# Optimization experiments

Hardware: AMD Instinct MI355X
Metric: run time of the kernel (lower is better)

Reference implementation:

```python
import jax, jax.numpy as jnp
import numpy as np

D_MODEL = 2048
N_HEADS = 8
EXPAND_K = 1
EXPAND_V = 2
DK = D_MODEL * EXPAND_K // N_HEADS      # 256 per-head key dim
DV = D_MODEL * EXPAND_V // N_HEADS      # 512 per-head value dim
INTER = 5632
EPS = 1e-6
CHUNK = 64


def setup_inputs() -> dict:
    key = jax.random.key(0)
    ks = jax.random.split(key, 12)
    d = D_MODEL
    s = lambda fan_in: 1.0 / np.sqrt(fan_in)
    return {
        "hidden_states": jax.random.normal(ks[0], (2, 2048, d), jnp.float32),
        "attn_norm_w": jnp.ones((d,), jnp.float32),
        "q_w": jax.random.normal(ks[1], (d, d * EXPAND_K), jnp.float32) * s(d),
        "k_w": jax.random.normal(ks[2], (d, d * EXPAND_K), jnp.float32) * s(d),
        "v_w": jax.random.normal(ks[3], (d, d * EXPAND_V), jnp.float32) * s(d),
        "g_w": jax.random.normal(ks[4], (d, d * EXPAND_V), jnp.float32) * s(d),
        "o_w": jax.random.normal(ks[5], (d * EXPAND_V, d), jnp.float32) * s(d * EXPAND_V),
        "gnorm_w": jnp.ones((DV,), jnp.float32),
        "mlp_norm_w": jnp.ones((d,), jnp.float32),
        "gate_w": jax.random.normal(ks[6], (d, INTER * 2), jnp.float32) * s(d),
        "down_w": jax.random.normal(ks[7], (INTER, d), jnp.float32) * s(INTER),
    }


def rmsnorm(x, w, eps=EPS):
    return x * jax.lax.rsqrt(jnp.mean(x * x, axis=-1, keepdims=True) + eps) * w


def rope(x):
    # x: [B, T, H, D]; non-interleaved rotary on full head dim
    T, D = x.shape[1], x.shape[-1]
    inv_freq = 1.0 / (10000.0 ** (jnp.arange(0, D, 2, dtype=jnp.float32) / D))
    ang = jnp.arange(T, dtype=jnp.float32)[:, None] * inv_freq  # [T, D/2]
    cos = jnp.cos(ang)[None, :, None, :]
    sin = jnp.sin(ang)[None, :, None, :]
    x1, x2 = jnp.split(x, 2, axis=-1)
    return jnp.concatenate([x1 * cos - x2 * sin, x2 * cos + x1 * sin], axis=-1)


def chunk_retention(q, k, v):
    # q,k: [B,T,H,Dk], v: [B,T,H,Dv]; chunkwise-recurrent RetNet retention
    B, T, H, Dk = q.shape
    Dv = v.shape[-1]
    C = CHUNK
    N = T // C
    gamma = 1.0 - jnp.exp2(-5.0 - jnp.arange(H, dtype=jnp.float32))  # [H]
    i = jnp.arange(C, dtype=jnp.float32)
    diff = i[:, None] - i[None, :]
    Dmask = jnp.where(diff >= 0, gamma[:, None, None] ** diff, 0.0)   # [H,C,C]
    cross_decay = gamma[:, None] ** (i[None, :] + 1.0)                # [H,C]
    k_decay = gamma[:, None] ** (C - 1.0 - i[None, :])                # [H,C]
    chunk_decay = gamma ** C                                          # [H]

    # -> [N, B, H, C, D]
    to_chunks = lambda x: jnp.moveaxis(
        x.reshape(B, N, C, H, x.shape[-1]).transpose(0, 1, 3, 2, 4), 1, 0)
    qc, kc, vc = to_chunks(q), to_chunks(k), to_chunks(v)

    def body(S, inp):
        qb, kb, vb = inp  # [B,H,C,Dk/Dv]
        attn = jnp.einsum('bhid,bhjd->bhij', qb, kb) * Dmask
        o_intra = jnp.einsum('bhij,bhje->bhie', attn, vb)
        o_cross = jnp.einsum('bhid,bhde->bhie', qb * cross_decay[None, :, :, None], S)
        S = chunk_decay[None, :, None, None] * S + \
            jnp.einsum('bhid,bhie->bhde', kb * k_decay[None, :, :, None], vb)
        return S, o_intra + o_cross

    S0 = jnp.zeros((B, H, Dk, Dv), q.dtype)
    _, o = jax.lax.scan(body, S0, (qc, kc, vc))  # o: [N,B,H,C,Dv]
    return jnp.moveaxis(o, 0, 1).transpose(0, 1, 3, 2, 4).reshape(B, T, H, Dv)


def reference(hidden_states, attn_norm_w, q_w, k_w, v_w, g_w, o_w, gnorm_w,
              mlp_norm_w, gate_w, down_w):
    B, T, d = hidden_states.shape
    residual = hidden_states
    h = rmsnorm(hidden_states, attn_norm_w)

    # MultiScaleRetention
    q = (h @ q_w).reshape(B, T, N_HEADS, DK)
    k = (h @ k_w).reshape(B, T, N_HEADS, DK)
    v = (h @ v_w).reshape(B, T, N_HEADS, DV)
    g = (h @ g_w).reshape(B, T, N_HEADS, DV)
    q, k = rope(q), rope(k)
    q = q * (DK ** -0.5)
    o = chunk_retention(q, k, v)
    # fused RMSNorm + swish gate (per head over Dv)
    o = rmsnorm(o, gnorm_w) * (g * jax.nn.sigmoid(g))
    h = o.reshape(B, T, N_HEADS * DV) @ o_w

    # fused-residual RMSNorm
    residual = h + residual
    h = rmsnorm(residual, mlp_norm_w)

    # SwiGLU MLP
    y = h @ gate_w
    gate, y = jnp.split(y, 2, axis=-1)
    h = (gate * jax.nn.sigmoid(gate) * y) @ down_w
    return residual + h
```

## Files before the change

### kernel.cpp

```cpp
#include <hip/hip_runtime.h>
#include <cstdint>
#include <cstddef>

typedef unsigned short u16;
typedef __attribute__((ext_vector_type(4))) float f32x4;
typedef __attribute__((ext_vector_type(4))) unsigned int u32x4;

__device__ __forceinline__ float b2f(u16 u) {
  union { unsigned int i; float f; } x; x.i = ((unsigned int)u) << 16; return x.f;
}
__device__ __forceinline__ u16 f2b(float f) {
  union { float f; unsigned int i; } x; x.f = f;
  unsigned int i = x.i;
  i += 0x7fffu + ((i >> 16) & 1u);
  return (u16)(i >> 16);
}

__device__ __forceinline__ void mfma_bf16(f32x4& c, u32x4 a, u32x4 b) {
  asm("v_mfma_f32_16x16x32_bf16 %0, %1, %2, %0" : "+v"(c) : "v"(a), "v"(b));
}

__device__ __forceinline__ void async_ld16(const u16* g, u16* l) {
  typedef __attribute__((address_space(1))) const unsigned int GU;
  typedef __attribute__((address_space(3))) unsigned int LU;
  __builtin_amdgcn_global_load_lds((GU*)g, (LU*)l, 16, 0, 0);
}

__global__ __launch_bounds__(256)
void transpose_cast_kernel(const float* __restrict__ in, u16* __restrict__ out,
                           int K, int N, int ldin) {
  __shared__ float tile[64][65];
  const int nb = N >> 6;
  const int bk = blockIdx.x / nb, bn = blockIdx.x % nb;
  const int k0 = bk * 64, n0 = bn * 64;
  const int tid = threadIdx.x;
#pragma unroll
  for (int p = 0; p < 16; ++p) {
    int idx = p * 256 + tid;
    int r = idx >> 6, c = idx & 63;
    tile[r][c] = in[(size_t)(k0 + r) * ldin + n0 + c];
  }
  __syncthreads();
#pragma unroll
  for (int p = 0; p < 16; ++p) {
    int idx = p * 256 + tid;
    int r = idx >> 6, c = idx & 63;
    out[(size_t)(n0 + r) * K + k0 + c] = f2b(tile[c][r]);
  }
}

__global__ __launch_bounds__(256)
void transpose_k_kernel(const u16* __restrict__ kb, u16* __restrict__ kt) {
  __shared__ u16 tile[64][72];
  const int bid = blockIdx.x;
  const int dd = bid & 3, tt = (bid >> 2) & 31;
  const int h = (bid >> 7) & 7, b = bid >> 10;
  const int t0 = tt * 64, d0 = dd * 64;
  const int tid = threadIdx.x;
#pragma unroll
  for (int p = 0; p < 2; ++p) {
    int idx = p * 256 + tid;
    int r = idx >> 3, cq = (idx & 7) * 8;
    *(uint4*)&tile[r][cq] =
        *(const uint4*)&kb[(size_t)(b * 2048 + t0 + r) * 2048 + h * 256 + d0 + cq];
  }
  __syncthreads();
#pragma unroll
  for (int p = 0; p < 2; ++p) {
    int idx = p * 256 + tid;
    int r = idx >> 3, cq = (idx & 7) * 8;
    union { u16 h8[8]; uint4 v4; } o;
#pragma unroll
    for (int j = 0; j < 8; ++j) o.h8[j] = tile[cq + j][r];
    *(uint4*)&kt[((size_t)(b * 8 + h) * 256 + d0 + r) * 2048 + t0 + cq] = o.v4;
  }
}

__global__ __launch_bounds__(256)
void rmsnorm_cast_kernel(const float* __restrict__ x, const float* __restrict__ w,
                         u16* __restrict__ out) {
  const int row = blockIdx.x, tid = threadIdx.x;
  const float* xr = x + (size_t)row * 2048;
  float4 a = ((const float4*)xr)[tid * 2];
  float4 b = ((const float4*)xr)[tid * 2 + 1];
  float ss = a.x*a.x + a.y*a.y + a.z*a.z + a.w*a.w
           + b.x*b.x + b.y*b.y + b.z*b.z + b.w*b.w;
#pragma unroll
  for (int m = 32; m; m >>= 1) ss += __shfl_xor(ss, m);
  __shared__ float ps[4];
  if ((tid & 63) == 0) ps[tid >> 6] = ss;
  __syncthreads();
  const float sc = rsqrtf((ps[0] + ps[1] + ps[2] + ps[3]) * (1.0f / 2048.0f) + 1e-6f);
  const int base = tid * 8;
  const float vals[8] = {a.x, a.y, a.z, a.w, b.x, b.y, b.z, b.w};
  union { u16 h[8]; uint4 v4[2]; } o;
#pragma unroll
  for (int j = 0; j < 8; ++j) o.h[j] = f2b(vals[j] * sc * w[base + j]);
  *(uint4*)&out[(size_t)row * 2048 + base] = o.v4[0];
  *(uint4*)&out[(size_t)row * 2048 + base + 8] = o.v4[1];
}

__global__ __launch_bounds__(256)
void rmsnorm_bf16_kernel(const u16* __restrict__ x, const float* __restrict__ w,
                         u16* __restrict__ out) {
  const int row = blockIdx.x, tid = threadIdx.x;
  union { uint4 v4; u16 h[8]; } p;
  p.v4 = *(const uint4*)&x[(size_t)row * 2048 + tid * 8];
  float v[8];
  float ss = 0.f;
#pragma unroll
  for (int j = 0; j < 8; ++j) { v[j] = b2f(p.h[j]); ss += v[j] * v[j]; }
#pragma unroll
  for (int m = 32; m; m >>= 1) ss += __shfl_xor(ss, m);
  __shared__ float ps[4];
  if ((tid & 63) == 0) ps[tid >> 6] = ss;
  __syncthreads();
  const float sc = rsqrtf((ps[0] + ps[1] + ps[2] + ps[3]) * (1.0f / 2048.0f) + 1e-6f);
  union { u16 h[8]; uint4 v4; } o;
#pragma unroll
  for (int j = 0; j < 8; ++j) o.h[j] = f2b(v[j] * sc * w[tid * 8 + j]);
  *(uint4*)&out[(size_t)row * 2048 + tid * 8] = o.v4;
}

__global__ __launch_bounds__(256)
void rope_table_kernel(float* __restrict__ ct, float* __restrict__ st) {
  const int idx = blockIdx.x * 256 + threadIdx.x;
  const int t = idx >> 7, i = idx & 127;
  const float e = -(float)i * (0.0078125f * log2f(10000.0f));
  const float ang = (float)t * exp2f(e);
  ct[idx] = cosf(ang);
  st[idx] = sinf(ang);
}

__global__ __launch_bounds__(256)
void rope_apply_kernel(u16* __restrict__ x, const float* __restrict__ ct,
                       const float* __restrict__ st, float scale) {
  const int gid = blockIdx.x * 256 + threadIdx.x;
  const int r = gid >> 8;
  const int rem = gid & 255;
  const int h = rem >> 5;
  const int i4 = (rem & 31) * 4;
  const int t = r & 2047;
  const size_t o1 = (size_t)r * 2048 + h * 256 + i4;
  union { ushort4 v; u16 h4[4]; } p1, p2, q1, q2;
  p1.v = *(ushort4*)&x[o1];
  p2.v = *(ushort4*)&x[o1 + 128];
  const float4 c = *(const float4*)&ct[t * 128 + i4];
  const float4 s = *(const float4*)&st[t * 128 + i4];
  const float cc[4] = {c.x, c.y, c.z, c.w};
  const float sn[4] = {s.x, s.y, s.z, s.w};
#pragma unroll
  for (int j = 0; j < 4; ++j) {
    float x1 = b2f(p1.h4[j]), x2 = b2f(p2.h4[j]);
    q1.h4[j] = f2b((x1 * cc[j] - x2 * sn[j]) * scale);
    q2.h4[j] = f2b((x2 * cc[j] + x1 * sn[j]) * scale);
  }
  *(ushort4*)&x[o1] = q1.v;
  *(ushort4*)&x[o1 + 128] = q2.v;
}

template <int BM, int EPI>
__global__ __launch_bounds__(512, 2)
void gemm2(const u16* __restrict__ A, const u16* __restrict__ Bt,
           void* Cout, const float* fsrc, const u16* hsrc, int N, int K) {
  constexpr int MF = BM / 32;
  constexpr int WROWS = BM / 2;
  constexpr int LA = BM / 128;
  constexpr int SLOTA = BM * 32;
  constexpr int SLOTB = 256 * 32;
  constexpr int SLOT = SLOTA + SLOTB;
  constexpr int VM2 = 2 * (LA + 2);
  __shared__ __align__(16) u16 lds[4 * SLOT];

  const int tid = threadIdx.x;
  const int l = tid & 63, w = tid >> 6;
  const int lr = l & 15, hi = l >> 4;
  const int wm = w >> 2, wn = w & 3;
  const int nbn = N >> 8;
  int bid;
  { int cpx = (int)gridDim.x >> 3; int ob = blockIdx.x;
    bid = (ob & 7) * cpx + (ob >> 3); }
  const int bm = bid / nbn, bn = bid % nbn;
  const int nt = K >> 5;

  size_t asrc[LA]; int adst[LA];
#pragma unroll
  for (int t = 0; t < LA; ++t) {
    int gi = t * 512 + tid;
    int row = gi >> 2;
    int ch = (gi & 3) ^ (row & 3);
    asrc[t] = (size_t)(bm * BM + row) * K + ch * 8;
    adst[t] = (t * 512 + w * 64) * 8;
  }
  size_t bsrc[2]; int bdst[2];
#pragma unroll
  for (int t = 0; t < 2; ++t) {
    int gi = t * 512 + tid;
    int row = gi >> 2;
    int ch = (gi & 3) ^ (row & 3);
    bsrc[t] = (size_t)(bn * 256 + row) * K + ch * 8;
    bdst[t] = SLOTA + (t * 512 + w * 64) * 8;
  }
  const int xch = (hi ^ (lr & 3)) << 3;
  int aoff[MF], boff[4];
#pragma unroll
  for (int m = 0; m < MF; ++m)
    aoff[m] = (wm * WROWS + m * 16 + lr) * 32 + xch;
#pragma unroll
  for (int n = 0; n < 4; ++n)
    boff[n] = SLOTA + (wn * 64 + n * 16 + lr) * 32 + xch;

  f32x4 acc[MF][4];
#pragma unroll
  for (int m = 0; m < MF; ++m)
#pragma unroll
    for (int n = 0; n < 4; ++n) acc[m][n] = (f32x4){0.f, 0.f, 0.f, 0.f};

  auto stage = [&](int kt, int s) {
    const int sb = s * SLOT;
#pragma unroll
    for (int t = 0; t < LA; ++t)
      async_ld16(A + (asrc[t] + kt * 32), &lds[sb + adst[t]]);
#pragma unroll
    for (int t = 0; t < 2; ++t)
      async_ld16(Bt + (bsrc[t] + kt * 32), &lds[sb + bdst[t]]);
  };

  stage(0, 0); __builtin_amdgcn_sched_barrier(0);
  stage(1, 1); __builtin_amdgcn_sched_barrier(0);
  stage(2, 2); __builtin_amdgcn_sched_barrier(0);
  asm volatile("s_waitcnt vmcnt(%0)" :: "n"(VM2) : "memory");
  __builtin_amdgcn_sched_barrier(0);
  __builtin_amdgcn_s_barrier();
  __builtin_amdgcn_sched_barrier(0);

  for (int i = 0; i < nt; ++i) {
    int pf = i + 3; if (pf >= nt) pf -= nt;
    stage(pf, (i + 3) & 3);
    __builtin_amdgcn_sched_barrier(0);
    const int sb = (i & 3) * SLOT;
    u32x4 af[MF], bf[4];
#pragma unroll
    for (int m = 0; m < MF; ++m) af[m] = *(const u32x4*)&lds[sb + aoff[m]];
#pragma unroll
    for (int n = 0; n < 4; ++n) bf[n] = *(const u32x4*)&lds[sb + boff[n]];
    __builtin_amdgcn_s_setprio(1);
#pragma unroll
    for (int m = 0; m < MF; ++m)
#pragma unroll
      for (int n = 0; n < 4; ++n) mfma_bf16(acc[m][n], af[m], bf[n]);
    __builtin_amdgcn_s_setprio(0);
    __builtin_amdgcn_sched_barrier(0);
    asm volatile("s_waitcnt vmcnt(%0)" :: "n"(VM2) : "memory");
    __builtin_amdgcn_sched_barrier(0);
    __builtin_amdgcn_s_barrier();
    __builtin_amdgcn_sched_barrier(0);
  }

  const size_t crow0 = (size_t)(bm * BM + wm * WROWS);
  const int ccol0 = bn * 256 + wn * 64;
#pragma unroll
  for (int m = 0; m < MF; ++m)
#pragma unroll
    for (int n = 0; n < 4; ++n)
#pragma unroll
      for (int j = 0; j < 4; ++j) {
        size_t r = crow0 + m * 16 + hi * 4 + j;
        size_t c = (size_t)(ccol0 + n * 16 + lr);
        size_t idx = r * N + c;
        float a = acc[m][n][j];
        if (EPI == 1) {
          ((u16*)Cout)[idx] = f2b(a);
        } else if (EPI == 2) {
          ((float*)Cout)[idx] = a + b2f(hsrc[idx]);
        } else if (EPI == 3) {
          float u = b2f(hsrc[idx]);
          ((u16*)Cout)[idx] = f2b(a / (1.0f + expf(-a)) * u);
        } else {
          ((u16*)Cout)[idx] = f2b(a + fsrc[idx]);
        }
      }
}

#define LGK 264
#define LGC 72
__global__ __launch_bounds__(512)
void retention_kernel(const u16* __restrict__ q, const u16* __restrict__ k,
                      const u16* __restrict__ kt, const u16* __restrict__ v,
                      u16* __restrict__ o) {
  __shared__ __align__(16) u16 ks[64 * LGK];
  __shared__ __align__(16) u16 stb[32 * LGK];
  __shared__ __align__(16) u16 ktd[256 * LGC];
  __shared__ __align__(16) u16 vts[32 * LGC];
  __shared__ __align__(16) u16 ab[64 * LGC];
  __shared__ float kdt[64];

  const int tid = threadIdx.x;
  const int l = tid & 63, w = tid >> 6;
  const int lr = l & 15, hi = l >> 4;
  const int wr = w >> 1;
  const int eb = w & 1;
  const int bid = blockIdx.x;
  const int g = bid & 15;
  const int sl = bid >> 4;
  const int hh = g & 7;
  const int b = g >> 3;
  const float gamma = 1.0f - exp2f(-5.0f - (float)hh);
  const float lg = log2f(gamma);
  const float cdk = exp2f(64.0f * lg);
  const int e0 = sl * 32;

  if (tid < 64) kdt[tid] = exp2f((float)(63 - tid) * lg);
  __syncthreads();

  f32x4 st[4];
#pragma unroll
  for (int t = 0; t < 4; ++t) st[t] = (f32x4){0.f, 0.f, 0.f, 0.f};

  for (int n = 0; n < 32; ++n) {
    const int row0 = b * 2048 + n * 64;
    const int t0 = n * 64;
#pragma unroll
    for (int t = 0; t < 4; ++t)
#pragma unroll
      for (int j = 0; j < 4; ++j)
        stb[(eb * 16 + hi * 4 + j) * LGK + (wr * 4 + t) * 16 + lr] = f2b(st[t][j]);
    u32x4 qf[8];
#pragma unroll
    for (int kk = 0; kk < 8; ++kk)
      qf[kk] = *(const u32x4*)&q[(size_t)(row0 + wr * 16 + lr) * 2048 +
                                 hh * 256 + kk * 32 + hi * 8];
#pragma unroll
    for (int p = 0; p < 4; ++p) {
      int idx = p * 512 + tid;
      int c = idx >> 5, s = (idx & 31) * 8;
      *(uint4*)&ks[c * LGK + s] =
          *(const uint4*)&k[(size_t)(row0 + c) * 2048 + hh * 256 + s];
    }
#pragma unroll
    for (int p = 0; p < 4; ++p) {
      int idx = p * 512 + tid;
      int d = idx >> 3, cq = (idx & 7) * 8;
      union { uint4 v4; u16 h[8]; } pk;
      pk.v4 = *(const uint4*)&kt[((size_t)(b * 8 + hh) * 256 + d) * 2048 + t0 + cq];
      union { u16 h[8]; uint4 v4; } wo;
#pragma unroll
      for (int j2 = 0; j2 < 8; ++j2)
        wo.h[j2] = f2b(b2f(pk.h[j2]) * kdt[cq + j2]);
      *(uint4*)&ktd[d * LGC + cq] = wo.v4;
    }
#pragma unroll
    for (int p = 0; p < 4; ++p) {
      int c = (tid >> 5) + p * 16, e = tid & 31;
      vts[e * LGC + c] = v[(size_t)(row0 + c) * 4096 + hh * 512 + e0 + e];
    }
    __syncthreads();

    f32x4 att[2];
    att[0] = (f32x4){0.f, 0.f, 0.f, 0.f};
    att[1] = (f32x4){0.f, 0.f, 0.f, 0.f};
#pragma unroll
    for (int kk = 0; kk < 8; ++kk) {
#pragma unroll
      for (int jf = 0; jf < 2; ++jf) {
        u32x4 bb = *(const u32x4*)&ks[(eb * 32 + jf * 16 + lr) * LGK + kk * 32 + hi * 8];
        mfma_bf16(att[jf], qf[kk], bb);
      }
    }
#pragma unroll
    for (int jf = 0; jf < 2; ++jf)
#pragma unroll
      for (int j = 0; j < 4; ++j) {
        int i = wr * 16 + hi * 4 + j;
        int jc = eb * 32 + jf * 16 + lr;
        float mv = (i >= jc) ? exp2f((float)(i - jc) * lg) : 0.0f;
        ab[i * LGC + jc] = f2b(att[jf][j] * mv);
      }
    f32x4 occ = (f32x4){0.f, 0.f, 0.f, 0.f};
#pragma unroll
    for (int kk = 0; kk < 8; ++kk) {
      u32x4 bb = *(const u32x4*)&stb[(eb * 16 + lr) * LGK + kk * 32 + hi * 8];
      mfma_bf16(occ, qf[kk], bb);
    }
    __syncthreads();

#pragma unroll
    for (int j = 0; j < 4; ++j) {
      int i = wr * 16 + hi * 4 + j;
      occ[j] *= exp2f((float)(i + 1) * lg);
    }
#pragma unroll
    for (int kk = 0; kk < 2; ++kk) {
      u32x4 aa = *(const u32x4*)&ab[(wr * 16 + lr) * LGC + kk * 32 + hi * 8];
      u32x4 bb = *(const u32x4*)&vts[(eb * 16 + lr) * LGC + kk * 32 + hi * 8];
      mfma_bf16(occ, aa, bb);
    }
#pragma unroll
    for (int j = 0; j < 4; ++j) {
      int i = wr * 16 + hi * 4 + j;
      o[(size_t)(row0 + i) * 4096 + hh * 512 + e0 + eb * 16 + lr] = f2b(occ[j]);
    }
#pragma unroll
    for (int t = 0; t < 4; ++t) {
      st[t][0] *= cdk; st[t][1] *= cdk; st[t][2] *= cdk; st[t][3] *= cdk;
    }
#pragma unroll
    for (int kk = 0; kk < 2; ++kk) {
      u32x4 aa = *(const u32x4*)&vts[(eb * 16 + lr) * LGC + kk * 32 + hi * 8];
#pragma unroll
      for (int t = 0; t < 4; ++t) {
        u32x4 bb = *(const u32x4*)&ktd[((wr * 4 + t) * 16 + lr) * LGC + kk * 32 + hi * 8];
        mfma_bf16(st[t], aa, bb);
      }
    }
    __syncthreads();
  }
}

__global__ __launch_bounds__(64)
void gating_kernel(u16* __restrict__ o, const u16* __restrict__ g,
                   const float* __restrict__ gnw) {
  const int blk = blockIdx.x;
  const size_t base = (size_t)blk * 512;
  const int l = threadIdx.x;
  union { uint4 v4; u16 h[8]; } ov, gv;
  ov.v4 = *(const uint4*)&o[base + l * 8];
  float x[8];
  float ss = 0.f;
#pragma unroll
  for (int j = 0; j < 8; ++j) { x[j] = b2f(ov.h[j]); ss += x[j] * x[j]; }
#pragma unroll
  for (int m = 32; m; m >>= 1) ss += __shfl_xor(ss, m);
  const float sc = rsqrtf(ss * (1.0f / 512.0f) + 1e-6f);
  gv.v4 = *(const uint4*)&g[base + l * 8];
  union { u16 h[8]; uint4 v4; } ou;
#pragma unroll
  for (int j = 0; j < 8; ++j) {
    float gvf = b2f(gv.h[j]);
    float sig = 1.0f / (1.0f + expf(-gvf));
    ou.h[j] = f2b(x[j] * sc * gnw[l * 8 + j] * gvf * sig);
  }
  *(uint4*)&o[base + l * 8] = ou.v4;
}

extern "C" void kernel_launch(void* const* d_in, const int* in_sizes, int n_in,
                              void* d_out, int out_size, void* d_ws, size_t ws_size,
                              hipStream_t stream) {
  (void)in_sizes; (void)n_in; (void)out_size; (void)ws_size;
  const float* hidden      = (const float*)d_in[0];
  const float* attn_norm_w = (const float*)d_in[1];
  const float* q_w         = (const float*)d_in[2];
  const float* k_w         = (const float*)d_in[3];
  const float* v_w         = (const float*)d_in[4];
  const float* g_w         = (const float*)d_in[5];
  const float* o_w         = (const float*)d_in[6];
  const float* gnorm_w     = (const float*)d_in[7];
  const float* mlp_norm_w  = (const float*)d_in[8];
  const float* gate_w      = (const float*)d_in[9];
  const float* down_w      = (const float*)d_in[10];
  float* outp = (float*)d_out;

  char* ws = (char*)d_ws;
  size_t off = 0;
  auto alloc = [&](size_t bytes) -> char* {
    char* p = ws + off;
    off += (bytes + 255) & ~(size_t)255;
    return p;
  };
  u16*   W    = (u16*)alloc(23068672ULL);
  float* ctab = (float*)alloc(1048576ULL);
  float* stab = (float*)alloc(1048576ULL);
  u16*   hb   = (u16*)alloc(16777216ULL);
  u16*   qb   = (u16*)alloc(16777216ULL);
  u16*   kb   = (u16*)alloc(16777216ULL);
  u16*   vb   = (u16*)alloc(33554432ULL);
  u16*   gb   = (u16*)alloc(33554432ULL);
  u16*   ob   = (u16*)alloc(33554432ULL);
  u16*   resb = (u16*)alloc(16777216ULL);
  u16*   ybU  = vb;
  u16*   kt   = W;

  rope_table_kernel<<<1024, 256, 0, stream>>>(ctab, stab);
  rmsnorm_cast_kernel<<<4096, 256, 0, stream>>>(hidden, attn_norm_w, hb);

  transpose_cast_kernel<<<1024, 256, 0, stream>>>(q_w, W, 2048, 2048, 2048);
  gemm2<128, 1><<<256, 512, 0, stream>>>(hb, W, (void*)qb, nullptr, nullptr, 2048, 2048);
  transpose_cast_kernel<<<1024, 256, 0, stream>>>(k_w, W, 2048, 2048, 2048);
  gemm2<128, 1><<<256, 512, 0, stream>>>(hb, W, (void*)kb, nullptr, nullptr, 2048, 2048);
  transpose_cast_kernel<<<2048, 256, 0, stream>>>(v_w, W, 2048, 4096, 4096);
  gemm2<256, 1><<<256, 512, 0, stream>>>(hb, W, (void*)vb, nullptr, nullptr, 4096, 2048);
  transpose_cast_kernel<<<2048, 256, 0, stream>>>(g_w, W, 2048, 4096, 4096);
  gemm2<256, 1><<<256, 512, 0, stream>>>(hb, W, (void*)gb, nullptr, nullptr, 4096, 2048);

  rope_apply_kernel<<<4096, 256, 0, stream>>>(qb, ctab, stab, 0.0625f);
  rope_apply_kernel<<<4096, 256, 0, stream>>>(kb, ctab, stab, 1.0f);
  transpose_k_kernel<<<2048, 256, 0, stream>>>(kb, kt);

  retention_kernel<<<256, 512, 0, stream>>>(qb, kb, kt, vb, ob);

  gating_kernel<<<32768, 64, 0, stream>>>(ob, gb, gnorm_w);

  transpose_cast_kernel<<<2048, 256, 0, stream>>>(o_w, W, 4096, 2048, 2048);
  gemm2<128, 4><<<256, 512, 0, stream>>>(ob, W, (void*)resb, hidden, nullptr, 2048, 4096);

  rmsnorm_bf16_kernel<<<4096, 256, 0, stream>>>(resb, mlp_norm_w, hb);

  transpose_cast_kernel<<<2816, 256, 0, stream>>>(gate_w + 5632, W, 2048, 5632, 11264);
  gemm2<128, 1><<<704, 512, 0, stream>>>(hb, W, (void*)ybU, nullptr, nullptr, 5632, 2048);
  transpose_cast_kernel<<<2816, 256, 0, stream>>>(gate_w, W, 2048, 5632, 11264);
  gemm2<128, 3><<<704, 512, 0, stream>>>(hb, W, (void*)ybU, nullptr, ybU, 5632, 2048);

  transpose_cast_kernel<<<2816, 256, 0, stream>>>(down_w, W, 5632, 2048, 2048);
  gemm2<128, 2><<<256, 512, 0, stream>>>(ybU, W, (void*)outp, nullptr, resb, 2048, 5632);
}
```

Measured before the change: 961.0 us.

## Fuse Q/K projections, add XCD-aware tile mapping and split-phase GEMM pipeline

Concatenates the transposed Q and K weights so one 256-row-tile GEMM produces an interleaved QK buffer, and updates rope, transpose and retention to read it with a 4096 stride. Replaces gemm2 with gemm3, which maps blocks to XCD-local rectangular tile groups for L2 reuse and uses a new LDS swizzle. For BM=256 it splits each k-step into two MFMA halves with extra barriers so prefetch overlaps compute. The MLP gate/up GEMMs move from 128 to 256 row tiles, halving their grid. The risks are more barriers per iteration and fewer blocks for load balance.

```diff
diff --git a/kernel.cpp b/kernel.cpp
--- a/kernel.cpp
+++ b/kernel.cpp
@@ -50,7 +50,7 @@
 }
 
 __global__ __launch_bounds__(256)
-void transpose_k_kernel(const u16* __restrict__ kb, u16* __restrict__ kt) {
+void transpose_k_kernel(const u16* __restrict__ qk, u16* __restrict__ kt) {
   __shared__ u16 tile[64][72];
   const int bid = blockIdx.x;
   const int dd = bid & 3, tt = (bid >> 2) & 31;
@@ -62,7 +62,7 @@
     int idx = p * 256 + tid;
     int r = idx >> 3, cq = (idx & 7) * 8;
     *(uint4*)&tile[r][cq] =
-        *(const uint4*)&kb[(size_t)(b * 2048 + t0 + r) * 2048 + h * 256 + d0 + cq];
+        *(const uint4*)&qk[(size_t)(b * 2048 + t0 + r) * 4096 + 2048 + h * 256 + d0 + cq];
   }
   __syncthreads();
 #pragma unroll
@@ -134,14 +134,14 @@
 
 __global__ __launch_bounds__(256)
 void rope_apply_kernel(u16* __restrict__ x, const float* __restrict__ ct,
-                       const float* __restrict__ st, float scale) {
+                       const float* __restrict__ st, int qoff, float scale) {
   const int gid = blockIdx.x * 256 + threadIdx.x;
   const int r = gid >> 8;
   const int rem = gid & 255;
   const int h = rem >> 5;
   const int i4 = (rem & 31) * 4;
   const int t = r & 2047;
-  const size_t o1 = (size_t)r * 2048 + h * 256 + i4;
+  const size_t o1 = (size_t)r * 4096 + qoff + h * 256 + i4;
   union { ushort4 v; u16 h4[4]; } p1, p2, q1, q2;
   p1.v = *(ushort4*)&x[o1];
   p2.v = *(ushort4*)&x[o1 + 128];
@@ -161,114 +161,136 @@
 
 template <int BM, int EPI>
 __global__ __launch_bounds__(512, 2)
-void gemm2(const u16* __restrict__ A, const u16* __restrict__ Bt,
-           void* Cout, const float* fsrc, const u16* hsrc, int N, int K) {
+void gemm3(const u16* __restrict__ A, const u16* __restrict__ Bt,
+           void* Cout, const float* fsrc, const u16* hsrc,
+           int N, int K, int lda, int pm, int pn, int gw) {
   constexpr int MF = BM / 32;
-  constexpr int WROWS = BM / 2;
+  constexpr int AS16 = BM * 4;
+  constexpr int SLOT16 = AS16 + 1024;
   constexpr int LA = BM / 128;
-  constexpr int SLOTA = BM * 32;
-  constexpr int SLOTB = 256 * 32;
-  constexpr int SLOT = SLOTA + SLOTB;
-  constexpr int VM2 = 2 * (LA + 2);
-  __shared__ __align__(16) u16 lds[4 * SLOT];
+  constexpr int VMC = 2 * (LA + 2);
+  __shared__ __align__(16) u16 lds[4 * SLOT16 * 8];
 
   const int tid = threadIdx.x;
   const int l = tid & 63, w = tid >> 6;
   const int lr = l & 15, hi = l >> 4;
   const int wm = w >> 2, wn = w & 3;
-  const int nbn = N >> 8;
-  int bid;
-  { int cpx = (int)gridDim.x >> 3; int ob = blockIdx.x;
-    bid = (ob & 7) * cpx + (ob >> 3); }
-  const int bm = bid / nbn, bn = bid % nbn;
+  const int xcd = blockIdx.x & 7;
+  const int j = blockIdx.x >> 3;
+  const int gx = xcd % gw, gy = xcd / gw;
+  const int bm = gx * pm + j / pn;
+  const int bn = gy * pn + j % pn;
   const int nt = K >> 5;
 
-  size_t asrc[LA]; int adst[LA];
+  const u16* Ap[LA]; const u16* Bp[2];
 #pragma unroll
   for (int t = 0; t < LA; ++t) {
-    int gi = t * 512 + tid;
-    int row = gi >> 2;
-    int ch = (gi & 3) ^ (row & 3);
-    asrc[t] = (size_t)(bm * BM + row) * K + ch * 8;
-    adst[t] = (t * 512 + w * 64) * 8;
-  }
-  size_t bsrc[2]; int bdst[2];
+    int s = t * 512 + tid;
+    int row = s >> 2, chL = (s & 3) ^ ((s >> 3) & 3);
+    Ap[t] = A + (size_t)(bm * BM + row) * lda + chL * 8;
+  }
 #pragma unroll
   for (int t = 0; t < 2; ++t) {
-    int gi = t * 512 + tid;
-    int row = gi >> 2;
-    int ch = (gi & 3) ^ (row & 3);
-    bsrc[t] = (size_t)(bn * 256 + row) * K + ch * 8;
-    bdst[t] = SLOTA + (t * 512 + w * 64) * 8;
-  }
-  const int xch = (hi ^ (lr & 3)) << 3;
+    int s = t * 512 + tid;
+    int row = s >> 2, chL = (s & 3) ^ ((s >> 3) & 3);
+    Bp[t] = Bt + (size_t)(bn * 256 + row) * K + chL * 8;
+  }
   int aoff[MF], boff[4];
 #pragma unroll
+  for (int mf = 0; mf < MF; ++mf) {
+    int r = wm * (BM / 2) + mf * 16 + lr;
+    aoff[mf] = r * 4 + (hi ^ ((r >> 1) & 3));
+  }
+#pragma unroll
+  for (int nf = 0; nf < 4; ++nf) {
+    int r = wn * 64 + nf * 16 + lr;
+    boff[nf] = AS16 + r * 4 + (hi ^ ((r >> 1) & 3));
+  }
+
+  f32x4 acc[MF][4];
+#pragma unroll
   for (int m = 0; m < MF; ++m)
-    aoff[m] = (wm * WROWS + m * 16 + lr) * 32 + xch;
-#pragma unroll
-  for (int n = 0; n < 4; ++n)
-    boff[n] = SLOTA + (wn * 64 + n * 16 + lr) * 32 + xch;
-
-  f32x4 acc[MF][4];
-#pragma unroll
-  for (int m = 0; m < MF; ++m)
 #pragma unroll
     for (int n = 0; n < 4; ++n) acc[m][n] = (f32x4){0.f, 0.f, 0.f, 0.f};
 
-  auto stage = [&](int kt, int s) {
-    const int sb = s * SLOT;
+#pragma unroll
+  for (int tt = 0; tt < 3; ++tt) {
+    const int sb = tt * SLOT16;
 #pragma unroll
     for (int t = 0; t < LA; ++t)
-      async_ld16(A + (asrc[t] + kt * 32), &lds[sb + adst[t]]);
+      async_ld16(Ap[t] + tt * 32, &lds[(size_t)(sb + t * 512 + w * 64) * 8]);
 #pragma unroll
     for (int t = 0; t < 2; ++t)
-      async_ld16(Bt + (bsrc[t] + kt * 32), &lds[sb + bdst[t]]);
-  };
-
-  stage(0, 0); __builtin_amdgcn_sched_barrier(0);
-  stage(1, 1); __builtin_amdgcn_sched_barrier(0);
-  stage(2, 2); __builtin_amdgcn_sched_barrier(0);
-  asm volatile("s_waitcnt vmcnt(%0)" :: "n"(VM2) : "memory");
+      async_ld16(Bp[t] + tt * 32, &lds[(size_t)(sb + AS16 + t * 512 + w * 64) * 8]);
+    __builtin_amdgcn_sched_barrier(0);
+  }
+  asm volatile("s_waitcnt vmcnt(%0)" :: "n"(VMC) : "memory");
   __builtin_amdgcn_sched_barrier(0);
   __builtin_amdgcn_s_barrier();
   __builtin_amdgcn_sched_barrier(0);
 
   for (int i = 0; i < nt; ++i) {
     int pf = i + 3; if (pf >= nt) pf -= nt;
-    stage(pf, (i + 3) & 3);
+    const int sc = (i & 3) * SLOT16;
+    const int sp = ((i + 3) & 3) * SLOT16;
+    u32x4 bf[4], af[4];
+#pragma unroll
+    for (int nf = 0; nf < 4; ++nf) bf[nf] = *(const u32x4*)&lds[(size_t)(sc + boff[nf]) * 8];
+#pragma unroll
+    for (int mf = 0; mf < 4; ++mf) af[mf] = *(const u32x4*)&lds[(size_t)(sc + aoff[mf]) * 8];
+#pragma unroll
+    for (int t = 0; t < LA; ++t)
+      async_ld16(Ap[t] + pf * 32, &lds[(size_t)(sp + t * 512 + w * 64) * 8]);
+    if (MF == 4) {
+#pragma unroll
+      for (int t = 0; t < 2; ++t)
+        async_ld16(Bp[t] + pf * 32, &lds[(size_t)(sp + AS16 + t * 512 + w * 64) * 8]);
+    }
     __builtin_amdgcn_sched_barrier(0);
-    const int sb = (i & 3) * SLOT;
-    u32x4 af[MF], bf[4];
-#pragma unroll
-    for (int m = 0; m < MF; ++m) af[m] = *(const u32x4*)&lds[sb + aoff[m]];
-#pragma unroll
-    for (int n = 0; n < 4; ++n) bf[n] = *(const u32x4*)&lds[sb + boff[n]];
+    __builtin_amdgcn_s_barrier();
     __builtin_amdgcn_s_setprio(1);
 #pragma unroll
-    for (int m = 0; m < MF; ++m)
-#pragma unroll
-      for (int n = 0; n < 4; ++n) mfma_bf16(acc[m][n], af[m], bf[n]);
+    for (int mf = 0; mf < 4; ++mf)
+#pragma unroll
+      for (int nf = 0; nf < 4; ++nf) mfma_bf16(acc[mf][nf], af[mf], bf[nf]);
     __builtin_amdgcn_s_setprio(0);
     __builtin_amdgcn_sched_barrier(0);
-    asm volatile("s_waitcnt vmcnt(%0)" :: "n"(VM2) : "memory");
+    if (MF == 8) {
+      __builtin_amdgcn_s_barrier();
+#pragma unroll
+      for (int mf = 0; mf < 4; ++mf)
+        af[mf] = *(const u32x4*)&lds[(size_t)(sc + aoff[4 + mf]) * 8];
+#pragma unroll
+      for (int t = 0; t < 2; ++t)
+        async_ld16(Bp[t] + pf * 32, &lds[(size_t)(sp + AS16 + t * 512 + w * 64) * 8]);
+      __builtin_amdgcn_sched_barrier(0);
+      __builtin_amdgcn_s_barrier();
+      __builtin_amdgcn_s_setprio(1);
+#pragma unroll
+      for (int mf = 0; mf < 4; ++mf)
+#pragma unroll
+        for (int nf = 0; nf < 4; ++nf) mfma_bf16(acc[4 + mf][nf], af[mf], bf[nf]);
+      __builtin_amdgcn_s_setprio(0);
+      __builtin_amdgcn_sched_barrier(0);
+    }
+    asm volatile("s_waitcnt vmcnt(%0)" :: "n"(VMC) : "memory");
     __builtin_amdgcn_sched_barrier(0);
     __builtin_amdgcn_s_barrier();
     __builtin_amdgcn_sched_barrier(0);
   }
 
-  const size_t crow0 = (size_t)(bm * BM + wm * WROWS);
+  const size_t crow0 = (size_t)(bm * BM + wm * (BM / 2));
   const int ccol0 = bn * 256 + wn * 64;
 #pragma unroll
   for (int m = 0; m < MF; ++m)
 #pragma unroll
     for (int n = 0; n < 4; ++n)
 #pragma unroll
-      for (int j = 0; j < 4; ++j) {
-        size_t r = crow0 + m * 16 + hi * 4 + j;
+      for (int j2 = 0; j2 < 4; ++j2) {
+        size_t r = crow0 + m * 16 + hi * 4 + j2;
         size_t c = (size_t)(ccol0 + n * 16 + lr);
         size_t idx = r * N + c;
-        float a = acc[m][n][j];
+        float a = acc[m][n][j2];
         if (EPI == 1) {
           ((u16*)Cout)[idx] = f2b(a);
         } else if (EPI == 2) {
@@ -285,9 +307,8 @@
 #define LGK 264
 #define LGC 72
 __global__ __launch_bounds__(512)
-void retention_kernel(const u16* __restrict__ q, const u16* __restrict__ k,
-                      const u16* __restrict__ kt, const u16* __restrict__ v,
-                      u16* __restrict__ o) {
+void retention_kernel(const u16* __restrict__ qk, const u16* __restrict__ kt,
+                      const u16* __restrict__ v, u16* __restrict__ o) {
   __shared__ __align__(16) u16 ks[64 * LGK];
   __shared__ __align__(16) u16 stb[32 * LGK];
   __shared__ __align__(16) u16 ktd[256 * LGC];
@@ -328,14 +349,14 @@
     u32x4 qf[8];
 #pragma unroll
     for (int kk = 0; kk < 8; ++kk)
-      qf[kk] = *(const u32x4*)&q[(size_t)(row0 + wr * 16 + lr) * 2048 +
-                                 hh * 256 + kk * 32 + hi * 8];
+      qf[kk] = *(const u32x4*)&qk[(size_t)(row0 + wr * 16 + lr) * 4096 +
+                                  hh * 256 + kk * 32 + hi * 8];
 #pragma unroll
     for (int p = 0; p < 4; ++p) {
       int idx = p * 512 + tid;
       int c = idx >> 5, s = (idx & 31) * 8;
       *(uint4*)&ks[c * LGK + s] =
-          *(const uint4*)&k[(size_t)(row0 + c) * 2048 + hh * 256 + s];
+          *(const uint4*)&qk[(size_t)(row0 + c) * 4096 + 2048 + hh * 256 + s];
     }
 #pragma unroll
     for (int p = 0; p < 4; ++p) {
@@ -471,45 +492,50 @@
   float* ctab = (float*)alloc(1048576ULL);
   float* stab = (float*)alloc(1048576ULL);
   u16*   hb   = (u16*)alloc(16777216ULL);
-  u16*   qb   = (u16*)alloc(16777216ULL);
-  u16*   kb   = (u16*)alloc(16777216ULL);
+  u16*   qkb  = (u16*)alloc(33554432ULL);
   u16*   vb   = (u16*)alloc(33554432ULL);
   u16*   gb   = (u16*)alloc(33554432ULL);
   u16*   ob   = (u16*)alloc(33554432ULL);
   u16*   resb = (u16*)alloc(16777216ULL);
-  u16*   ybU  = vb;
+  u16*   ybU  = qkb;
   u16*   kt   = W;
 
   rope_table_kernel<<<1024, 256, 0, stream>>>(ctab, stab);
   rmsnorm_cast_kernel<<<4096, 256, 0, stream>>>(hidden, attn_norm_w, hb);
 
   transpose_cast_kernel<<<1024, 256, 0, stream>>>(q_w, W, 2048, 2048, 2048);
-  gemm2<128, 1><<<256, 512, 0, stream>>>(hb, W, (void*)qb, nullptr, nullptr, 2048, 2048);
-  transpose_cast_kernel<<<1024, 256, 0, stream>>>(k_w, W, 2048, 2048, 2048);
-  gemm2<128, 1><<<256, 512, 0, stream>>>(hb, W, (void*)kb, nullptr, nullptr, 2048, 2048);
+  transpose_cast_kernel<<<1024, 256, 0, stream>>>(k_w, W + 2048ULL * 2048, 2048, 2048, 2048);
+  gemm3<256, 1><<<256, 512, 0, stream>>>(hb, W, (void*)qkb, nullptr, nullptr,
+                                         4096, 2048, 2048, 8, 4, 2);
   transpose_cast_kernel<<<2048, 256, 0, stream>>>(v_w, W, 2048, 4096, 4096);
-  gemm2<256, 1><<<256, 512, 0, stream>>>(hb, W, (void*)vb, nullptr, nullptr, 4096, 2048);
+  gemm3<256, 1><<<256, 512, 0, stream>>>(hb, W, (void*)vb, nullptr, nullptr,
+                                         4096, 2048, 2048, 8, 4, 2);
   transpose_cast_kernel<<<2048, 256, 0, stream>>>(g_w, W, 2048, 4096, 4096);
-  gemm2<256, 1><<<256, 512, 0, stream>>>(hb, W, (void*)gb, nullptr, nullptr, 4096, 2048);
-
-  rope_apply_kernel<<<4096, 256, 0, stream>>>(qb, ctab, stab, 0.0625f);
-  rope_apply_kernel<<<4096, 256, 0, stream>>>(kb, ctab, stab, 1.0f);
-  transpose_k_kernel<<<2048, 256, 0, stream>>>(kb, kt);
-
-  retention_kernel<<<256, 512, 0, stream>>>(qb, kb, kt, vb, ob);
+  gemm3<256, 1><<<256, 512, 0, stream>>>(hb, W, (void*)gb, nullptr, nullptr,
+                                         4096, 2048, 2048, 8, 4, 2);
+
+  rope_apply_kernel<<<4096, 256, 0, stream>>>(qkb, ctab, stab, 0, 0.0625f);
+  rope_apply_kernel<<<4096, 256, 0, stream>>>(qkb, ctab, stab, 2048, 1.0f);
+  transpose_k_kernel<<<2048, 256, 0, stream>>>(qkb, kt);
+
+  retention_kernel<<<256, 512, 0, stream>>>(qkb, kt, vb, ob);
 
   gating_kernel<<<32768, 64, 0, stream>>>(ob, gb, gnorm_w);
 
   transpose_cast_kernel<<<2048, 256, 0, stream>>>(o_w, W, 4096, 2048, 2048);
-  gemm2<128, 4><<<256, 512, 0, stream>>>(ob, W, (void*)resb, hidden, nullptr, 2048, 4096);
+  gemm3<128, 4><<<256, 512, 0, stream>>>(ob, W, (void*)resb, hidden, nullptr,
+                                         2048, 4096, 4096, 8, 4, 4);
 
   rmsnorm_bf16_kernel<<<4096, 256, 0, stream>>>(resb, mlp_norm_w, hb);
 
   transpose_cast_kernel<<<2816, 256, 0, stream>>>(gate_w + 5632, W, 2048, 5632, 11264);
-  gemm2<128, 1><<<704, 512, 0, stream>>>(hb, W, (void*)ybU, nullptr, nullptr, 5632, 2048);
+  gemm3<256, 1><<<352, 512, 0, stream>>>(hb, W, (void*)ybU, nullptr, nullptr,
+                                         5632, 2048, 2048, 4, 11, 4);
   transpose_cast_kernel<<<2816, 256, 0, stream>>>(gate_w, W, 2048, 5632, 11264);
-  gemm2<128, 3><<<704, 512, 0, stream>>>(hb, W, (void*)ybU, nullptr, ybU, 5632, 2048);
+  gemm3<256, 3><<<352, 512, 0, stream>>>(hb, W, (void*)ybU, nullptr, ybU,
+                                         5632, 2048, 2048, 4, 11, 4);
 
   transpose_cast_kernel<<<2816, 256, 0, stream>>>(down_w, W, 5632, 2048, 2048);
-  gemm2<128, 2><<<256, 512, 0, stream>>>(ybU, W, (void*)outp, nullptr, resb, 2048, 5632);
-}
+  gemm3<128, 2><<<256, 512, 0, stream>>>(ybU, W, (void*)outp, nullptr, resb,
+                                         2048, 5632, 5632, 8, 4, 4);
+}
```

Measured after the change: 963.5 us. No clear change (+0.3%).
